# Optimization experiments

Measured on AMD Instinct MI355X. Metric: run time of the kernel, lower is better.

## Reference

```python
import jax, jax.numpy as jnp
import numpy as np

NUM_ITER = 10  # torch forward default num_iter=10


def _normalize_rows(x):
    # x / (||x||_2 per row + 1e-6), matching torch data.norm(dim=1)[:, None]
    return x / (jnp.linalg.norm(x, axis=1, keepdims=True) + 1e-6)


def _cluster(data, init, cluster_temp, num_iter):
    # Soft k-means: normalize data once, then iterate
    # mu-normalize -> cosine sim -> softmax assignments -> weighted mean update.
    data = _normalize_rows(data)           # [N, D]
    mu = init                              # [K, D]
    dist = None
    for _ in range(num_iter):
        mu_n = _normalize_rows(mu)         # [K, D]
        dist = data @ mu_n.T               # [N, K]
        r = jax.nn.softmax(cluster_temp * dist, axis=1)  # [N, K]
        # diag(1/r.sum(0)) @ (r.T @ data) == row-wise divide
        mu = (r.T @ data) / r.sum(axis=0)[:, None]       # [K, D]
    r = jax.nn.softmax(cluster_temp * dist, axis=1)
    return mu, r


def setup_inputs() -> dict:
    key = jax.random.key(0)
    k1, k2 = jax.random.split(key)
    N, D, K = 100000, 512, 256
    embeds = jax.random.normal(k1, (N, D), dtype=jnp.float32)
    # self.init = torch.rand(K, nout): uniform [0, 1)
    init = jax.random.uniform(k2, (K, D), dtype=jnp.float32)
    cluster_temp = jnp.float32(30.0)
    return {"embeds": embeds, "cluster_temp": cluster_temp, "init": init}


def reference(embeds, cluster_temp, init):
    # First pass: 10 iterations from random init; result is detached in torch.
    mu_init, _ = _cluster(embeds, init, cluster_temp, NUM_ITER)
    mu_init = jax.lax.stop_gradient(mu_init)
    # Second pass: single iteration from detached means (grad flows here).
    mu, r = _cluster(embeds, mu_init, cluster_temp, 1)
    return mu, r
```

## Files before the change

### kernel.cpp

```cpp
#include <hip/hip_runtime.h>
#include <math.h>


#define DIMD 512
#define KCL 256
#define NSPLIT 96

typedef __attribute__((ext_vector_type(8))) short short8;
typedef __attribute__((ext_vector_type(4))) short short4v;
typedef __attribute__((ext_vector_type(4))) float float4v;

__device__ __forceinline__ short f2bf(float x) {
  union { float f; unsigned u; } v; v.f = x;
  unsigned r = v.u + 0x7fff + ((v.u >> 16) & 1);
  return (short)(r >> 16);
}
__device__ __forceinline__ float bf2f(short b) {
  union { unsigned u; float f; } v;
  v.u = ((unsigned)(unsigned short)b) << 16;
  return v.f;
}

__global__ void row_norms_k(const float* __restrict__ x,
                            float* __restrict__ inv_norm, int n) {
  int wave = threadIdx.x >> 6;
  int lane = threadIdx.x & 63;
  int row = blockIdx.x * 4 + wave;
  if (row >= n) return;
  const float4* xr = (const float4*)(x + (size_t)row * DIMD);
  float4 a = xr[lane];
  float4 b = xr[lane + 64];
  float s = a.x*a.x + a.y*a.y + a.z*a.z + a.w*a.w
          + b.x*b.x + b.y*b.y + b.z*b.z + b.w*b.w;
#pragma unroll
  for (int m = 32; m >= 1; m >>= 1) s += __shfl_xor(s, m);
  if (lane == 0) inv_norm[row] = 1.0f / (sqrtf(s) + 1e-6f);
}

__global__ void mu_norm_k(const float* __restrict__ mu_src,
                          const float* __restrict__ colsum_in,
                          short* __restrict__ mu_hi, short* __restrict__ mu_lo,
                          float* __restrict__ mu_acc_z,
                          float* __restrict__ colsum_z, int use_colsum) {
  int k = blockIdx.x;
  int t = threadIdx.x;
  float inv_c = 1.0f;
  if (use_colsum) inv_c = 1.0f / colsum_in[k];
  float v0 = mu_src[k * DIMD + t] * inv_c;
  float v1 = mu_src[k * DIMD + t + 256] * inv_c;
  float s = v0 * v0 + v1 * v1;
#pragma unroll
  for (int m = 32; m >= 1; m >>= 1) s += __shfl_xor(s, m);
  __shared__ float sred[4];
  int lane = t & 63, wv = t >> 6;
  if (lane == 0) sred[wv] = s;
  __syncthreads();
  s = sred[0] + sred[1] + sred[2] + sred[3];
  float inv = 1.0f / (sqrtf(s) + 1e-6f);
  float w0 = v0 * inv, w1 = v1 * inv;
  short h0 = f2bf(w0), h1 = f2bf(w1);
  mu_hi[k * DIMD + t] = h0;
  mu_hi[k * DIMD + t + 256] = h1;
  mu_lo[k * DIMD + t] = f2bf(w0 - bf2f(h0));
  mu_lo[k * DIMD + t + 256] = f2bf(w1 - bf2f(h1));
  mu_acc_z[k * DIMD + t] = 0.0f;
  mu_acc_z[k * DIMD + t + 256] = 0.0f;
  if (t == 0) colsum_z[k] = 0.0f;
}

__global__ void final_mu_k(const float* __restrict__ mu_acc,
                           const float* __restrict__ colsum,
                           float* __restrict__ out) {
  int k = blockIdx.x;
  int t = threadIdx.x;
  float ic = 1.0f / colsum[k];
  out[k * DIMD + t] = mu_acc[k * DIMD + t] * ic;
  out[k * DIMD + t + 256] = mu_acc[k * DIMD + t + 256] * ic;
}

__global__ __launch_bounds__(256) void dist_mfma_k(
    const float* __restrict__ data, const float* __restrict__ inv_norm,
    const short* __restrict__ mu_hi, const short* __restrict__ mu_lo,
    unsigned* __restrict__ r_pack, float* __restrict__ r_f32, int write_f32,
    float* __restrict__ colsum, const float* __restrict__ temp_p, int n) {
  __shared__ __align__(16) short a_lds[64][72];
  __shared__ __align__(16) short b_lds[256][72];
  __shared__ __align__(16) float red[64][4];

  int t = threadIdx.x;
  int wave = t >> 6, lane = t & 63, q = lane >> 4, lx = lane & 15;
  int i0 = blockIdx.x * 64;

  float4v acc[4][4];
#pragma unroll
  for (int mt = 0; mt < 4; ++mt)
#pragma unroll
    for (int nt = 0; nt < 4; ++nt) acc[mt][nt] = (float4v)0.0f;

  for (int ch = 0; ch < 16; ++ch) {
    int d0 = ch * 32;
    {
      int row = t >> 2, seg = t & 3;
      int gi = i0 + row;
      if (gi > n - 1) gi = n - 1;
      const float* p = data + (size_t)gi * DIMD + d0 + seg * 8;
      float4 x0 = *(const float4*)p;
      float4 x1 = *(const float4*)(p + 4);
      float sc = inv_norm[gi];
      float vv[8] = {x0.x * sc, x0.y * sc, x0.z * sc, x0.w * sc,
                     x1.x * sc, x1.y * sc, x1.z * sc, x1.w * sc};
      short8 hv, lv;
#pragma unroll
      for (int j = 0; j < 8; ++j) {
        short h = f2bf(vv[j]);
        hv[j] = h;
        lv[j] = f2bf(vv[j] - bf2f(h));
      }
      *(short8*)&a_lds[row][seg * 8] = hv;
      *(short8*)&a_lds[row][32 + seg * 8] = lv;
    }
    {
      int seg = t & 3, kb = t >> 2;
#pragma unroll
      for (int rep = 0; rep < 4; ++rep) {
        int k = rep * 64 + kb;
        short8 h = *(const short8*)(mu_hi + (size_t)k * DIMD + d0 + seg * 8);
        short8 l = *(const short8*)(mu_lo + (size_t)k * DIMD + d0 + seg * 8);
        *(short8*)&b_lds[k][seg * 8] = h;
        *(short8*)&b_lds[k][32 + seg * 8] = l;
      }
    }
    __syncthreads();
    short8 ah[4], al[4], bh[4], bl[4];
#pragma unroll
    for (int mt = 0; mt < 4; ++mt) {
      ah[mt] = *(const short8*)&a_lds[mt * 16 + lx][q * 8];
      al[mt] = *(const short8*)&a_lds[mt * 16 + lx][32 + q * 8];
    }
#pragma unroll
    for (int nt = 0; nt < 4; ++nt) {
      int kr = wave * 64 + nt * 16 + lx;
      bh[nt] = *(const short8*)&b_lds[kr][q * 8];
      bl[nt] = *(const short8*)&b_lds[kr][32 + q * 8];
    }
#pragma unroll
    for (int mt = 0; mt < 4; ++mt)
#pragma unroll
      for (int nt = 0; nt < 4; ++nt) {
        acc[mt][nt] = __builtin_amdgcn_mfma_f32_16x16x32_bf16(
            ah[mt], bh[nt], acc[mt][nt], 0, 0, 0);
        acc[mt][nt] = __builtin_amdgcn_mfma_f32_16x16x32_bf16(
            ah[mt], bl[nt], acc[mt][nt], 0, 0, 0);
        acc[mt][nt] = __builtin_amdgcn_mfma_f32_16x16x32_bf16(
            al[mt], bh[nt], acc[mt][nt], 0, 0, 0);
      }
    __syncthreads();
  }

  float tempv = temp_p[0];
  float rs[4][4];
#pragma unroll
  for (int mt = 0; mt < 4; ++mt)
#pragma unroll
    for (int reg = 0; reg < 4; ++reg) {
      float s = 0.0f;
#pragma unroll
      for (int nt = 0; nt < 4; ++nt) {
        float e = __expf(tempv * acc[mt][nt][reg]);
        acc[mt][nt][reg] = e;
        s += e;
      }
      s += __shfl_xor(s, 1);
      s += __shfl_xor(s, 2);
      s += __shfl_xor(s, 4);
      s += __shfl_xor(s, 8);
      rs[mt][reg] = s;
    }
  if (lx == 0) {
#pragma unroll
    for (int mt = 0; mt < 4; ++mt)
#pragma unroll
      for (int reg = 0; reg < 4; ++reg)
        red[mt * 16 + q * 4 + reg][wave] = rs[mt][reg];
  }
  __syncthreads();

  float cs[4] = {0.0f, 0.0f, 0.0f, 0.0f};
#pragma unroll
  for (int mt = 0; mt < 4; ++mt)
#pragma unroll
    for (int reg = 0; reg < 4; ++reg) {
      int row = mt * 16 + q * 4 + reg;
      float4 v = *(const float4*)&red[row][0];
      float is = 1.0f / (v.x + v.y + v.z + v.w);
      int gi = i0 + row;
      bool ok = gi < n;
#pragma unroll
      for (int nt = 0; nt < 4; ++nt) {
        float r = acc[mt][nt][reg] * is;
        acc[mt][nt][reg] = r;
        if (ok) cs[nt] += r;
      }
      if (ok) {
        if (write_f32) {
#pragma unroll
          for (int nt = 0; nt < 4; ++nt)
            r_f32[(size_t)gi * KCL + wave * 64 + nt * 16 + lx] =
                acc[mt][nt][reg];
        } else {
#pragma unroll
          for (int nt = 0; nt < 4; ++nt) {
            float r = acc[mt][nt][reg];
            short h = f2bf(r);
            short l = f2bf(r - bf2f(h));
            r_pack[(size_t)gi * KCL + wave * 64 + nt * 16 + lx] =
                ((unsigned)(unsigned short)h << 16) | (unsigned short)l;
          }
        }
      }
    }
#pragma unroll
  for (int nt = 0; nt < 4; ++nt) {
    cs[nt] += __shfl_xor(cs[nt], 16);
    cs[nt] += __shfl_xor(cs[nt], 32);
  }
  if (q == 0) {
#pragma unroll
    for (int nt = 0; nt < 4; ++nt)
      atomicAdd(&colsum[wave * 64 + nt * 16 + lx], cs[nt]);
  }
}

__global__ __launch_bounds__(256) void update_mfma_k(
    const unsigned* __restrict__ r_src, int r_is_f32,
    const float* __restrict__ data, const float* __restrict__ inv_norm,
    float* __restrict__ mu_acc, int n) {
  __shared__ __align__(16) short rT[128][72];
  __shared__ __align__(16) short xT[128][72];

  int t = threadIdx.x, wave = t >> 6, lane = t & 63, q = lane >> 4,
      lx = lane & 15;
  int bx = blockIdx.x;
  int k0 = (bx & 1) * 128, d0 = (bx >> 1) * 128;
  int ns = blockIdx.y;
  int chunk = (n + NSPLIT - 1) / NSPLIT;
  int ibeg = ns * chunk;
  int iend = ibeg + chunk;
  if (iend > n) iend = n;
  int wk = wave >> 1, wd = wave & 1;
  int iq = t >> 5, kq = t & 31;

  float4v acc[4][4];
#pragma unroll
  for (int mt = 0; mt < 4; ++mt)
#pragma unroll
    for (int nt = 0; nt < 4; ++nt) acc[mt][nt] = (float4v)0.0f;

  for (int ib = ibeg; ib < iend; ib += 32) {
    {
      short h[4][4], l[4][4];
#pragma unroll
      for (int ii = 0; ii < 4; ++ii) {
        int gi = ib + iq * 4 + ii;
        uint4 u = make_uint4(0u, 0u, 0u, 0u);
        if (gi < iend)
          u = *(const uint4*)(r_src + (size_t)gi * KCL + k0 + kq * 4);
        unsigned uu[4] = {u.x, u.y, u.z, u.w};
        if (r_is_f32) {
#pragma unroll
          for (int kk = 0; kk < 4; ++kk) {
            union { unsigned u; float f; } c; c.u = uu[kk];
            short hh = f2bf(c.f);
            h[ii][kk] = hh;
            l[ii][kk] = f2bf(c.f - bf2f(hh));
          }
        } else {
#pragma unroll
          for (int kk = 0; kk < 4; ++kk) {
            h[ii][kk] = (short)(uu[kk] >> 16);
            l[ii][kk] = (short)(uu[kk] & 0xffffu);
          }
        }
      }
#pragma unroll
      for (int kk = 0; kk < 4; ++kk) {
        short4v vh = {h[0][kk], h[1][kk], h[2][kk], h[3][kk]};
        short4v vl = {l[0][kk], l[1][kk], l[2][kk], l[3][kk]};
        *(short4v*)&rT[kq * 4 + kk][iq * 4] = vh;
        *(short4v*)&rT[kq * 4 + kk][32 + iq * 4] = vl;
      }
    }
    {
      short h[4][4], l[4][4];
#pragma unroll
      for (int ii = 0; ii < 4; ++ii) {
        int gi = ib + iq * 4 + ii;
        float4 x = make_float4(0.f, 0.f, 0.f, 0.f);
        float sc = 0.0f;
        if (gi < iend) {
          x = *(const float4*)(data + (size_t)gi * DIMD + d0 + kq * 4);
          sc = inv_norm[gi];
        }
        float vv[4] = {x.x * sc, x.y * sc, x.z * sc, x.w * sc};
#pragma unroll
        for (int kk = 0; kk < 4; ++kk) {
          short hh = f2bf(vv[kk]);
          h[ii][kk] = hh;
          l[ii][kk] = f2bf(vv[kk] - bf2f(hh));
        }
      }
#pragma unroll
      for (int kk = 0; kk < 4; ++kk) {
        short4v vh = {h[0][kk], h[1][kk], h[2][kk], h[3][kk]};
        short4v vl = {l[0][kk], l[1][kk], l[2][kk], l[3][kk]};
        *(short4v*)&xT[kq * 4 + kk][iq * 4] = vh;
        *(short4v*)&xT[kq * 4 + kk][32 + iq * 4] = vl;
      }
    }
    __syncthreads();
    short8 ah[4], al[4], bh[4], bl[4];
#pragma unroll
    for (int mt = 0; mt < 4; ++mt) {
      int kr = wk * 64 + mt * 16 + lx;
      ah[mt] = *(const short8*)&rT[kr][q * 8];
      al[mt] = *(const short8*)&rT[kr][32 + q * 8];
    }
#pragma unroll
    for (int nt = 0; nt < 4; ++nt) {
      int dr = wd * 64 + nt * 16 + lx;
      bh[nt] = *(const short8*)&xT[dr][q * 8];
      bl[nt] = *(const short8*)&xT[dr][32 + q * 8];
    }
#pragma unroll
    for (int mt = 0; mt < 4; ++mt)
#pragma unroll
      for (int nt = 0; nt < 4; ++nt) {
        acc[mt][nt] = __builtin_amdgcn_mfma_f32_16x16x32_bf16(
            ah[mt], bh[nt], acc[mt][nt], 0, 0, 0);
        acc[mt][nt] = __builtin_amdgcn_mfma_f32_16x16x32_bf16(
            ah[mt], bl[nt], acc[mt][nt], 0, 0, 0);
        acc[mt][nt] = __builtin_amdgcn_mfma_f32_16x16x32_bf16(
            al[mt], bh[nt], acc[mt][nt], 0, 0, 0);
      }
    __syncthreads();
  }
#pragma unroll
  for (int mt = 0; mt < 4; ++mt)
#pragma unroll
    for (int nt = 0; nt < 4; ++nt)
#pragma unroll
      for (int reg = 0; reg < 4; ++reg) {
        int k = k0 + wk * 64 + mt * 16 + q * 4 + reg;
        int d = d0 + wd * 64 + nt * 16 + lx;
        atomicAdd(&mu_acc[(size_t)k * DIMD + d], acc[mt][nt][reg]);
      }
}

extern "C" void kernel_launch(void* const* d_in, const int* in_sizes, int n_in,
                              void* d_out, int out_size, void* d_ws,
                              size_t ws_size, hipStream_t stream) {
  const float* embeds = (const float*)d_in[0];
  const float* temp_p = (const float*)d_in[1];
  const float* init = (const float*)d_in[2];
  int n = in_sizes[0] / DIMD;

  float* out_mu = (float*)d_out;
  float* out_r = (float*)d_out + KCL * DIMD;

  float* wsf = (float*)d_ws;
  float* inv_norm = wsf;
  float* mu_acc = wsf + ((n + 3) & ~3);
  float* colsum = mu_acc + KCL * DIMD;
  short* mu_hi = (short*)(colsum + 256);
  short* mu_lo = mu_hi + KCL * DIMD;

  row_norms_k<<<(n + 3) / 4, 256, 0, stream>>>(embeds, inv_norm, n);
  mu_norm_k<<<KCL, 256, 0, stream>>>(init, colsum, mu_hi, mu_lo, mu_acc,
                                     colsum, 0);

  for (int it = 0; it <= 10; ++it) {
    int wf32 = (it == 10) ? 1 : 0;
    dist_mfma_k<<<(n + 63) / 64, 256, 0, stream>>>(
        embeds, inv_norm, mu_hi, mu_lo, (unsigned*)out_r, out_r, wf32, colsum,
        temp_p, n);
    update_mfma_k<<<dim3(8, NSPLIT), 256, 0, stream>>>(
        (const unsigned*)out_r, wf32, embeds, inv_norm, mu_acc, n);
    if (it < 10) {
      mu_norm_k<<<KCL, 256, 0, stream>>>(mu_acc, colsum, mu_hi, mu_lo, mu_acc,
                                         colsum, 1);
    } else {
      final_mu_k<<<KCL, 256, 0, stream>>>(mu_acc, colsum, out_mu);
    }
  }
}
```

Baseline: 3.871 ms.

## Precompute bf16 hi/lo data planes and transposed layouts for dist and update GEMMs

Converts the normalized embeddings once into bf16 hi/lo planes, row-major and transposed, held in workspace. The distance kernel then loads MFMA fragments straight from global memory without LDS staging or per-iteration conversion. The assignment matrix is written transposed so a new update kernel streams both operands contiguously along N. This removes repeated fp32-to-bf16 splitting and LDS transposes in all eleven iterations, at the cost of extra workspace, a one-time transpose pass, and strided scattered writes of r. A tiered fallback keeps the old path when the workspace is too small.

```diff
diff --git a/kernel.cpp b/kernel.cpp
--- a/kernel.cpp
+++ b/kernel.cpp
@@ -5,6 +5,7 @@
 #define DIMD 512
 #define KCL 256
 #define NSPLIT 96
+#define NCH_V2 128
 
 typedef __attribute__((ext_vector_type(8))) short short8;
 typedef __attribute__((ext_vector_type(4))) short short4v;
@@ -21,20 +22,88 @@
   return v.f;
 }
 
-__global__ void row_norms_k(const float* __restrict__ x,
-                            float* __restrict__ inv_norm, int n) {
+__global__ void row_norms_conv_k(const float* __restrict__ x,
+                                 float* __restrict__ inv_norm,
+                                 short* __restrict__ pl_hi,
+                                 short* __restrict__ pl_lo, int n,
+                                 int do_planes) {
   int wave = threadIdx.x >> 6;
   int lane = threadIdx.x & 63;
   int row = blockIdx.x * 4 + wave;
   if (row >= n) return;
-  const float4* xr = (const float4*)(x + (size_t)row * DIMD);
-  float4 a = xr[lane];
-  float4 b = xr[lane + 64];
+  const float* p = x + (size_t)row * DIMD + lane * 8;
+  float4 a = *(const float4*)p;
+  float4 b = *(const float4*)(p + 4);
   float s = a.x*a.x + a.y*a.y + a.z*a.z + a.w*a.w
           + b.x*b.x + b.y*b.y + b.z*b.z + b.w*b.w;
 #pragma unroll
   for (int m = 32; m >= 1; m >>= 1) s += __shfl_xor(s, m);
-  if (lane == 0) inv_norm[row] = 1.0f / (sqrtf(s) + 1e-6f);
+  float inv = 1.0f / (sqrtf(s) + 1e-6f);
+  if (lane == 0) inv_norm[row] = inv;
+  if (do_planes) {
+    float vv[8] = {a.x*inv, a.y*inv, a.z*inv, a.w*inv,
+                   b.x*inv, b.y*inv, b.z*inv, b.w*inv};
+    short8 hv, lv;
+#pragma unroll
+    for (int j = 0; j < 8; ++j) {
+      short h = f2bf(vv[j]);
+      hv[j] = h;
+      lv[j] = f2bf(vv[j] - bf2f(h));
+    }
+    *(short8*)(pl_hi + (size_t)row * DIMD + lane * 8) = hv;
+    *(short8*)(pl_lo + (size_t)row * DIMD + lane * 8) = lv;
+  }
+}
+
+__global__ __launch_bounds__(256) void transpose_k(
+    const float* __restrict__ x, const float* __restrict__ inv_norm,
+    short* __restrict__ xT_hi, short* __restrict__ xT_lo, int n) {
+  __shared__ unsigned lds[64][65];
+  int t = threadIdx.x;
+  int i0 = blockIdx.x * 64, d0 = blockIdx.y * 64;
+  {
+    int il = t >> 2, seg = (t & 3) * 16;
+    int gi = i0 + il; if (gi > n - 1) gi = n - 1;
+    float sc = inv_norm[gi];
+    const float* p = x + (size_t)gi * DIMD + d0 + seg;
+    float4 f0 = *(const float4*)p;
+    float4 f1 = *(const float4*)(p + 4);
+    float4 f2 = *(const float4*)(p + 8);
+    float4 f3 = *(const float4*)(p + 12);
+    float vv[16] = {f0.x,f0.y,f0.z,f0.w, f1.x,f1.y,f1.z,f1.w,
+                    f2.x,f2.y,f2.z,f2.w, f3.x,f3.y,f3.z,f3.w};
+#pragma unroll
+    for (int j = 0; j < 16; ++j) {
+      float v = vv[j] * sc;
+      short h = f2bf(v);
+      short l = f2bf(v - bf2f(h));
+      lds[seg + j][il] =
+          ((unsigned)(unsigned short)h << 16) | (unsigned short)l;
+    }
+  }
+  __syncthreads();
+  {
+    int dl = t >> 2, isg = (t & 3) * 16;
+    if (i0 + isg < n) {
+      unsigned u[16];
+#pragma unroll
+      for (int j = 0; j < 16; ++j) u[j] = lds[dl][isg + j];
+      union S8u { short8 s; unsigned w[4]; };
+      S8u h0, h1, l0, l1;
+#pragma unroll
+      for (int j = 0; j < 4; ++j) {
+        h0.w[j] = __builtin_amdgcn_perm(u[2*j+1], u[2*j], 0x07060302u);
+        l0.w[j] = __builtin_amdgcn_perm(u[2*j+1], u[2*j], 0x05040100u);
+        h1.w[j] = __builtin_amdgcn_perm(u[2*j+9], u[2*j+8], 0x07060302u);
+        l1.w[j] = __builtin_amdgcn_perm(u[2*j+9], u[2*j+8], 0x05040100u);
+      }
+      size_t rb = (size_t)(d0 + dl) * n + i0 + isg;
+      *(short8*)(xT_hi + rb) = h0.s;
+      *(short8*)(xT_hi + rb + 8) = h1.s;
+      *(short8*)(xT_lo + rb) = l0.s;
+      *(short8*)(xT_lo + rb + 8) = l1.s;
+    }
+  }
 }
 
 __global__ void mu_norm_k(const float* __restrict__ mu_src,
@@ -78,13 +147,14 @@
   out[k * DIMD + t + 256] = mu_acc[k * DIMD + t + 256] * ic;
 }
 
-__global__ __launch_bounds__(256) void dist_mfma_k(
+template <int PRE, int TS>
+__global__ __launch_bounds__(256, 2) void dist_k(
     const float* __restrict__ data, const float* __restrict__ inv_norm,
+    const short* __restrict__ pl_hi, const short* __restrict__ pl_lo,
     const short* __restrict__ mu_hi, const short* __restrict__ mu_lo,
-    unsigned* __restrict__ r_pack, float* __restrict__ r_f32, int write_f32,
+    unsigned* __restrict__ r_pack, float* __restrict__ r_f32,
+    unsigned* __restrict__ rt_also, int write_f32,
     float* __restrict__ colsum, const float* __restrict__ temp_p, int n) {
-  __shared__ __align__(16) short a_lds[64][72];
-  __shared__ __align__(16) short b_lds[256][72];
   __shared__ __align__(16) float red[64][4];
 
   int t = threadIdx.x;
@@ -97,64 +167,110 @@
 #pragma unroll
     for (int nt = 0; nt < 4; ++nt) acc[mt][nt] = (float4v)0.0f;
 
-  for (int ch = 0; ch < 16; ++ch) {
-    int d0 = ch * 32;
-    {
-      int row = t >> 2, seg = t & 3;
-      int gi = i0 + row;
+  if constexpr (PRE) {
+    const short *aH[4], *aL[4], *bH[4], *bL[4];
+#pragma unroll
+    for (int mt = 0; mt < 4; ++mt) {
+      int gi = i0 + mt * 16 + lx;
       if (gi > n - 1) gi = n - 1;
-      const float* p = data + (size_t)gi * DIMD + d0 + seg * 8;
-      float4 x0 = *(const float4*)p;
-      float4 x1 = *(const float4*)(p + 4);
-      float sc = inv_norm[gi];
-      float vv[8] = {x0.x * sc, x0.y * sc, x0.z * sc, x0.w * sc,
-                     x1.x * sc, x1.y * sc, x1.z * sc, x1.w * sc};
-      short8 hv, lv;
-#pragma unroll
-      for (int j = 0; j < 8; ++j) {
-        short h = f2bf(vv[j]);
-        hv[j] = h;
-        lv[j] = f2bf(vv[j] - bf2f(h));
-      }
-      *(short8*)&a_lds[row][seg * 8] = hv;
-      *(short8*)&a_lds[row][32 + seg * 8] = lv;
-    }
-    {
-      int seg = t & 3, kb = t >> 2;
-#pragma unroll
-      for (int rep = 0; rep < 4; ++rep) {
-        int k = rep * 64 + kb;
-        short8 h = *(const short8*)(mu_hi + (size_t)k * DIMD + d0 + seg * 8);
-        short8 l = *(const short8*)(mu_lo + (size_t)k * DIMD + d0 + seg * 8);
-        *(short8*)&b_lds[k][seg * 8] = h;
-        *(short8*)&b_lds[k][32 + seg * 8] = l;
-      }
-    }
-    __syncthreads();
-    short8 ah[4], al[4], bh[4], bl[4];
-#pragma unroll
-    for (int mt = 0; mt < 4; ++mt) {
-      ah[mt] = *(const short8*)&a_lds[mt * 16 + lx][q * 8];
-      al[mt] = *(const short8*)&a_lds[mt * 16 + lx][32 + q * 8];
+      size_t o = (size_t)gi * DIMD + q * 8;
+      aH[mt] = pl_hi + o;
+      aL[mt] = pl_lo + o;
     }
 #pragma unroll
     for (int nt = 0; nt < 4; ++nt) {
-      int kr = wave * 64 + nt * 16 + lx;
-      bh[nt] = *(const short8*)&b_lds[kr][q * 8];
-      bl[nt] = *(const short8*)&b_lds[kr][32 + q * 8];
-    }
-#pragma unroll
-    for (int mt = 0; mt < 4; ++mt)
+      size_t o = (size_t)(wave * 64 + nt * 16 + lx) * DIMD + q * 8;
+      bH[nt] = mu_hi + o;
+      bL[nt] = mu_lo + o;
+    }
+#pragma unroll 2
+    for (int ch = 0; ch < 16; ++ch) {
+      int d0 = ch * 32;
+      short8 ah[4], al[4], bh[4], bl[4];
+#pragma unroll
+      for (int mt = 0; mt < 4; ++mt) {
+        ah[mt] = *(const short8*)(aH[mt] + d0);
+        al[mt] = *(const short8*)(aL[mt] + d0);
+      }
 #pragma unroll
       for (int nt = 0; nt < 4; ++nt) {
-        acc[mt][nt] = __builtin_amdgcn_mfma_f32_16x16x32_bf16(
-            ah[mt], bh[nt], acc[mt][nt], 0, 0, 0);
-        acc[mt][nt] = __builtin_amdgcn_mfma_f32_16x16x32_bf16(
-            ah[mt], bl[nt], acc[mt][nt], 0, 0, 0);
-        acc[mt][nt] = __builtin_amdgcn_mfma_f32_16x16x32_bf16(
-            al[mt], bh[nt], acc[mt][nt], 0, 0, 0);
-      }
-    __syncthreads();
+        bh[nt] = *(const short8*)(bH[nt] + d0);
+        bl[nt] = *(const short8*)(bL[nt] + d0);
+      }
+#pragma unroll
+      for (int mt = 0; mt < 4; ++mt)
+#pragma unroll
+        for (int nt = 0; nt < 4; ++nt) {
+          acc[mt][nt] = __builtin_amdgcn_mfma_f32_16x16x32_bf16(
+              ah[mt], bh[nt], acc[mt][nt], 0, 0, 0);
+          acc[mt][nt] = __builtin_amdgcn_mfma_f32_16x16x32_bf16(
+              ah[mt], bl[nt], acc[mt][nt], 0, 0, 0);
+          acc[mt][nt] = __builtin_amdgcn_mfma_f32_16x16x32_bf16(
+              al[mt], bh[nt], acc[mt][nt], 0, 0, 0);
+        }
+    }
+  } else {
+    __shared__ __align__(16) short a_lds[64][72];
+    __shared__ __align__(16) short b_lds[256][72];
+    for (int ch = 0; ch < 16; ++ch) {
+      int d0 = ch * 32;
+      {
+        int row = t >> 2, seg = t & 3;
+        int gi = i0 + row;
+        if (gi > n - 1) gi = n - 1;
+        const float* p = data + (size_t)gi * DIMD + d0 + seg * 8;
+        float4 x0 = *(const float4*)p;
+        float4 x1 = *(const float4*)(p + 4);
+        float sc = inv_norm[gi];
+        float vv[8] = {x0.x * sc, x0.y * sc, x0.z * sc, x0.w * sc,
+                       x1.x * sc, x1.y * sc, x1.z * sc, x1.w * sc};
+        short8 hv, lv;
+#pragma unroll
+        for (int j = 0; j < 8; ++j) {
+          short h = f2bf(vv[j]);
+          hv[j] = h;
+          lv[j] = f2bf(vv[j] - bf2f(h));
+        }
+        *(short8*)&a_lds[row][seg * 8] = hv;
+        *(short8*)&a_lds[row][32 + seg * 8] = lv;
+      }
+      {
+        int seg = t & 3, kb = t >> 2;
+#pragma unroll
+        for (int rep = 0; rep < 4; ++rep) {
+          int k = rep * 64 + kb;
+          short8 h = *(const short8*)(mu_hi + (size_t)k * DIMD + d0 + seg * 8);
+          short8 l = *(const short8*)(mu_lo + (size_t)k * DIMD + d0 + seg * 8);
+          *(short8*)&b_lds[k][seg * 8] = h;
+          *(short8*)&b_lds[k][32 + seg * 8] = l;
+        }
+      }
+      __syncthreads();
+      short8 ah[4], al[4], bh[4], bl[4];
+#pragma unroll
+      for (int mt = 0; mt < 4; ++mt) {
+        ah[mt] = *(const short8*)&a_lds[mt * 16 + lx][q * 8];
+        al[mt] = *(const short8*)&a_lds[mt * 16 + lx][32 + q * 8];
+      }
+#pragma unroll
+      for (int nt = 0; nt < 4; ++nt) {
+        int kr = wave * 64 + nt * 16 + lx;
+        bh[nt] = *(const short8*)&b_lds[kr][q * 8];
+        bl[nt] = *(const short8*)&b_lds[kr][32 + q * 8];
+      }
+#pragma unroll
+      for (int mt = 0; mt < 4; ++mt)
+#pragma unroll
+        for (int nt = 0; nt < 4; ++nt) {
+          acc[mt][nt] = __builtin_amdgcn_mfma_f32_16x16x32_bf16(
+              ah[mt], bh[nt], acc[mt][nt], 0, 0, 0);
+          acc[mt][nt] = __builtin_amdgcn_mfma_f32_16x16x32_bf16(
+              ah[mt], bl[nt], acc[mt][nt], 0, 0, 0);
+          acc[mt][nt] = __builtin_amdgcn_mfma_f32_16x16x32_bf16(
+              al[mt], bh[nt], acc[mt][nt], 0, 0, 0);
+        }
+      __syncthreads();
+    }
   }
 
   float tempv = temp_p[0];
@@ -207,14 +323,28 @@
           for (int nt = 0; nt < 4; ++nt)
             r_f32[(size_t)gi * KCL + wave * 64 + nt * 16 + lx] =
                 acc[mt][nt][reg];
+          if (rt_also) {
+#pragma unroll
+            for (int nt = 0; nt < 4; ++nt) {
+              float r = acc[mt][nt][reg];
+              short h = f2bf(r);
+              short l = f2bf(r - bf2f(h));
+              rt_also[(size_t)(wave * 64 + nt * 16 + lx) * n + gi] =
+                  ((unsigned)(unsigned short)h << 16) | (unsigned short)l;
+            }
+          }
         } else {
 #pragma unroll
           for (int nt = 0; nt < 4; ++nt) {
             float r = acc[mt][nt][reg];
             short h = f2bf(r);
             short l = f2bf(r - bf2f(h));
-            r_pack[(size_t)gi * KCL + wave * 64 + nt * 16 + lx] =
+            unsigned u =
                 ((unsigned)(unsigned short)h << 16) | (unsigned short)l;
+            if constexpr (TS)
+              r_pack[(size_t)(wave * 64 + nt * 16 + lx) * n + gi] = u;
+            else
+              r_pack[(size_t)gi * KCL + wave * 64 + nt * 16 + lx] = u;
           }
         }
       }
@@ -229,6 +359,87 @@
     for (int nt = 0; nt < 4; ++nt)
       atomicAdd(&colsum[wave * 64 + nt * 16 + lx], cs[nt]);
   }
+}
+
+__global__ __launch_bounds__(256, 2) void update_v2_k(
+    const unsigned* __restrict__ rT, const short* __restrict__ xT_hi,
+    const short* __restrict__ xT_lo, float* __restrict__ mu_acc, int n,
+    int chunk) {
+  int t = threadIdx.x, wave = t >> 6, lane = t & 63, q = lane >> 4,
+      lx = lane & 15;
+  int B = blockIdx.x;
+  int x = B & 7, m = B >> 3, tt = m & 7, g = m >> 3;
+  int c = x + 8 * g;
+  int ibeg = c * chunk;
+  if (ibeg >= n) return;
+  int iend = ibeg + chunk;
+  if (iend > n) iend = n;
+  int k0 = (tt & 1) * 128, d0 = (tt >> 1) * 128;
+  int wk = wave >> 1, wd = wave & 1;
+
+  const unsigned* abase[4];
+  const short* bhb[4];
+  const short* blb[4];
+#pragma unroll
+  for (int mt = 0; mt < 4; ++mt)
+    abase[mt] = rT + (size_t)(k0 + wk * 64 + mt * 16 + lx) * n + q * 8;
+#pragma unroll
+  for (int nt = 0; nt < 4; ++nt) {
+    size_t dr = (size_t)(d0 + wd * 64 + nt * 16 + lx) * n + q * 8;
+    bhb[nt] = xT_hi + dr;
+    blb[nt] = xT_lo + dr;
+  }
+
+  float4v acc[4][4];
+#pragma unroll
+  for (int mt = 0; mt < 4; ++mt)
+#pragma unroll
+    for (int nt = 0; nt < 4; ++nt) acc[mt][nt] = (float4v)0.0f;
+
+  union S8u { short8 s; unsigned w[4]; };
+  for (int ib = ibeg; ib < iend; ib += 32) {
+    short8 bh[4], bl[4];
+#pragma unroll
+    for (int nt = 0; nt < 4; ++nt) {
+      bh[nt] = *(const short8*)(bhb[nt] + ib);
+      bl[nt] = *(const short8*)(blb[nt] + ib);
+    }
+    S8u ah[4], al[4];
+#pragma unroll
+    for (int mt = 0; mt < 4; ++mt) {
+      uint4 p0 = *(const uint4*)(abase[mt] + ib);
+      uint4 p1 = *(const uint4*)(abase[mt] + ib + 4);
+      unsigned pp[8] = {p0.x, p0.y, p0.z, p0.w, p1.x, p1.y, p1.z, p1.w};
+#pragma unroll
+      for (int j = 0; j < 4; ++j) {
+        ah[mt].w[j] =
+            __builtin_amdgcn_perm(pp[2 * j + 1], pp[2 * j], 0x07060302u);
+        al[mt].w[j] =
+            __builtin_amdgcn_perm(pp[2 * j + 1], pp[2 * j], 0x05040100u);
+      }
+    }
+#pragma unroll
+    for (int mt = 0; mt < 4; ++mt)
+#pragma unroll
+      for (int nt = 0; nt < 4; ++nt) {
+        acc[mt][nt] = __builtin_amdgcn_mfma_f32_16x16x32_bf16(
+            ah[mt].s, bh[nt], acc[mt][nt], 0, 0, 0);
+        acc[mt][nt] = __builtin_amdgcn_mfma_f32_16x16x32_bf16(
+            ah[mt].s, bl[nt], acc[mt][nt], 0, 0, 0);
+        acc[mt][nt] = __builtin_amdgcn_mfma_f32_16x16x32_bf16(
+            al[mt].s, bh[nt], acc[mt][nt], 0, 0, 0);
+      }
+  }
+#pragma unroll
+  for (int mt = 0; mt < 4; ++mt)
+#pragma unroll
+    for (int nt = 0; nt < 4; ++nt)
+#pragma unroll
+      for (int reg = 0; reg < 4; ++reg) {
+        int k = k0 + wk * 64 + mt * 16 + q * 4 + reg;
+        int d = d0 + wd * 64 + nt * 16 + lx;
+        atomicAdd(&mu_acc[(size_t)k * DIMD + d], acc[mt][nt][reg]);
+      }
 }
 
 __global__ __launch_bounds__(256) void update_mfma_k(
@@ -269,10 +480,10 @@
         if (r_is_f32) {
 #pragma unroll
           for (int kk = 0; kk < 4; ++kk) {
-            union { unsigned u; float f; } c; c.u = uu[kk];
-            short hh = f2bf(c.f);
+            union { unsigned u; float f; } cvt; cvt.u = uu[kk];
+            short hh = f2bf(cvt.f);
             h[ii][kk] = hh;
-            l[ii][kk] = f2bf(c.f - bf2f(hh));
+            l[ii][kk] = f2bf(cvt.f - bf2f(hh));
           }
         } else {
 #pragma unroll
@@ -295,13 +506,13 @@
 #pragma unroll
       for (int ii = 0; ii < 4; ++ii) {
         int gi = ib + iq * 4 + ii;
-        float4 x = make_float4(0.f, 0.f, 0.f, 0.f);
+        float4 xx = make_float4(0.f, 0.f, 0.f, 0.f);
         float sc = 0.0f;
         if (gi < iend) {
-          x = *(const float4*)(data + (size_t)gi * DIMD + d0 + kq * 4);
+          xx = *(const float4*)(data + (size_t)gi * DIMD + d0 + kq * 4);
           sc = inv_norm[gi];
         }
-        float vv[4] = {x.x * sc, x.y * sc, x.z * sc, x.w * sc};
+        float vv[4] = {xx.x * sc, xx.y * sc, xx.z * sc, xx.w * sc};
 #pragma unroll
         for (int kk = 0; kk < 4; ++kk) {
           short hh = f2bf(vv[kk]);
@@ -365,30 +576,86 @@
   int n = in_sizes[0] / DIMD;
 
   float* out_mu = (float*)d_out;
-  float* out_r = (float*)d_out + KCL * DIMD;
-
-  float* wsf = (float*)d_ws;
-  float* inv_norm = wsf;
-  float* mu_acc = wsf + ((n + 3) & ~3);
-  float* colsum = mu_acc + KCL * DIMD;
-  short* mu_hi = (short*)(colsum + 256);
-  short* mu_lo = mu_hi + KCL * DIMD;
-
-  row_norms_k<<<(n + 3) / 4, 256, 0, stream>>>(embeds, inv_norm, n);
+  float* out_r = (float*)d_out + (size_t)KCL * DIMD;
+
+  char* base = (char*)d_ws;
+  size_t off = 0;
+  auto alloc = [&](size_t bytes) {
+    char* p = base + off;
+    off += (bytes + 255) & ~(size_t)255;
+    return p;
+  };
+  float* inv_norm = (float*)alloc((size_t)n * 4);
+  float* mu_acc = (float*)alloc((size_t)KCL * DIMD * 4);
+  float* colsum = (float*)alloc(1024);
+  short* mu_hi = (short*)alloc((size_t)KCL * DIMD * 2);
+  short* mu_lo = (short*)alloc((size_t)KCL * DIMD * 2);
+
+  const size_t PL = (size_t)n * DIMD * 2;
+  const size_t RTB = (size_t)n * KCL * 4;
+  const size_t SLACK = 4096;
+
+  short *xT_hi = nullptr, *xT_lo = nullptr, *pl_hi = nullptr, *pl_lo = nullptr;
+  unsigned* rT2 = nullptr;
+  int tier = 0;
+  if (off + 2 * PL + SLACK <= ws_size) {
+    xT_hi = (short*)alloc(PL);
+    xT_lo = (short*)alloc(PL);
+    tier = 1;
+  }
+  if (tier == 1 && off + 2 * PL + SLACK <= ws_size) {
+    pl_hi = (short*)alloc(PL);
+    pl_lo = (short*)alloc(PL);
+    tier = 2;
+  }
+  if (tier == 2 && off + RTB + SLACK <= ws_size) {
+    rT2 = (unsigned*)alloc(RTB);
+    tier = 3;
+  }
+
+  row_norms_conv_k<<<(n + 3) / 4, 256, 0, stream>>>(embeds, inv_norm, pl_hi,
+                                                    pl_lo, n, tier >= 2);
+  if (tier >= 1)
+    transpose_k<<<dim3((n + 63) / 64, DIMD / 64), 256, 0, stream>>>(
+        embeds, inv_norm, xT_hi, xT_lo, n);
   mu_norm_k<<<KCL, 256, 0, stream>>>(init, colsum, mu_hi, mu_lo, mu_acc,
                                      colsum, 0);
 
+  int chunk_v2 = (((n + NCH_V2 - 1) / NCH_V2) + 31) & ~31;
+  int dist_grid = (n + 63) / 64;
+
   for (int it = 0; it <= 10; ++it) {
     int wf32 = (it == 10) ? 1 : 0;
-    dist_mfma_k<<<(n + 63) / 64, 256, 0, stream>>>(
-        embeds, inv_norm, mu_hi, mu_lo, (unsigned*)out_r, out_r, wf32, colsum,
-        temp_p, n);
-    update_mfma_k<<<dim3(8, NSPLIT), 256, 0, stream>>>(
-        (const unsigned*)out_r, wf32, embeds, inv_norm, mu_acc, n);
+    unsigned* rta = (wf32 && tier >= 3) ? rT2 : nullptr;
+    if (tier >= 2)
+      dist_k<1, 1><<<dist_grid, 256, 0, stream>>>(
+          embeds, inv_norm, pl_hi, pl_lo, mu_hi, mu_lo, (unsigned*)out_r,
+          out_r, rta, wf32, colsum, temp_p, n);
+    else if (tier == 1)
+      dist_k<0, 1><<<dist_grid, 256, 0, stream>>>(
+          embeds, inv_norm, pl_hi, pl_lo, mu_hi, mu_lo, (unsigned*)out_r,
+          out_r, nullptr, wf32, colsum, temp_p, n);
+    else
+      dist_k<0, 0><<<dist_grid, 256, 0, stream>>>(
+          embeds, inv_norm, pl_hi, pl_lo, mu_hi, mu_lo, (unsigned*)out_r,
+          out_r, nullptr, wf32, colsum, temp_p, n);
+
     if (it < 10) {
+      if (tier >= 1)
+        update_v2_k<<<8 * NCH_V2, 256, 0, stream>>>(
+            (const unsigned*)out_r, xT_hi, xT_lo, mu_acc, n, chunk_v2);
+      else
+        update_mfma_k<<<dim3(8, NSPLIT), 256, 0, stream>>>(
+            (const unsigned*)out_r, 0, embeds, inv_norm, mu_acc, n);
       mu_norm_k<<<KCL, 256, 0, stream>>>(mu_acc, colsum, mu_hi, mu_lo, mu_acc,
                                          colsum, 1);
     } else {
+      if (tier >= 3)
+        update_v2_k<<<8 * NCH_V2, 256, 0, stream>>>(rT2, xT_hi, xT_lo, mu_acc,
+                                                    n, chunk_v2);
+      else
+        update_mfma_k<<<dim3(8, NSPLIT), 256, 0, stream>>>(
+            (const unsigned*)out_r, 1, embeds, inv_norm, mu_acc, n);
       final_mu_k<<<KCL, 256, 0, stream>>>(mu_acc, colsum, out_mu);
     }
   }
```

Result: slower. 5.903 ms (+52.5%).
